# Performance work log

Measured on AMD Instinct MI355X. Metric: run time of the kernel, lower is better.

Reference implementation:

```python
import jax, jax.numpy as jnp
import numpy as np
from jax import lax

CHAR_SIZE, EMBED, HID = 20000, 128, 256
B, T = 256, 512


def setup_inputs() -> dict:
    key = jax.random.key(0)
    ks = jax.random.split(key, 12)
    s = 0.02
    return {
        "inputs": jax.random.randint(ks[0], (B, T), 0, CHAR_SIZE, dtype=jnp.int32),
        "input_end": jax.random.randint(ks[1], (B,), 0, B, dtype=jnp.int32),
        "embed_table": jax.random.normal(ks[2], (CHAR_SIZE, EMBED), jnp.float32) * s,
        "Wf": jax.random.normal(ks[3], (EMBED, 4 * HID), jnp.float32) * s,
        "Uf": jax.random.normal(ks[4], (HID, 4 * HID), jnp.float32) * s,
        "bf": jnp.zeros((4 * HID,), jnp.float32),
        "Wb": jax.random.normal(ks[5], (EMBED, 4 * HID), jnp.float32) * s,
        "Ub": jax.random.normal(ks[6], (HID, 4 * HID), jnp.float32) * s,
        "bb": jnp.zeros((4 * HID,), jnp.float32),
        "cls_W": jax.random.normal(ks[7], (2 * HID, 1), jnp.float32) * s,
        "cls_b": jnp.zeros((1,), jnp.float32),
        "ent_W": jax.random.normal(ks[8], (2 * HID, 3), jnp.float32) * s,
        "ent_b": jnp.zeros((3,), jnp.float32),
    }


def _masked_lstm(x_tbe, m_tb, W, U, b, reverse):
    """Keras-style masked LSTM; returns final hidden state [B, H].
    Masked steps carry (h, c) through unchanged."""
    Bn = x_tbe.shape[1]
    H = U.shape[0]

    def step(carry, inp):
        h, c = carry
        xt, mt = inp  # xt: [B,E], mt: [B]
        z = xt @ W + h @ U + b  # [B, 4H]
        i, f, g, o = jnp.split(z, 4, axis=-1)
        c_new = jax.nn.sigmoid(f) * c + jax.nn.sigmoid(i) * jnp.tanh(g)
        h_new = jax.nn.sigmoid(o) * jnp.tanh(c_new)
        m = mt[:, None]
        return (jnp.where(m, h_new, h), jnp.where(m, c_new, c)), None

    init = (jnp.zeros((Bn, H), x_tbe.dtype), jnp.zeros((Bn, H), x_tbe.dtype))
    (h, _), _ = lax.scan(step, init, (x_tbe, m_tb), reverse=reverse)
    return h


def reference(inputs, input_end, embed_table, Wf, Uf, bf, Wb, Ub, bb,
              cls_W, cls_b, ent_W, ent_b):
    mask = inputs > 0  # [B, T]
    embed = embed_table[inputs]  # [B, T, E]
    x_tbe = jnp.swapaxes(embed, 0, 1)  # [T, B, E]
    m_tb = mask.T  # [T, B]
    h_fwd = _masked_lstm(x_tbe, m_tb, Wf, Uf, bf, reverse=False)  # [B, H]
    h_bwd = _masked_lstm(x_tbe, m_tb, Wb, Ub, bb, reverse=True)   # [B, H]
    bivalue = jnp.concatenate([h_fwd, h_bwd], axis=-1)  # [B, 2H]
    sentence_end = bivalue[input_end]  # gather along batch axis, as in the original
    classifier_logits = jax.nn.sigmoid(sentence_end @ cls_W + cls_b)  # [B, 1]
    entity_logits = jax.nn.softmax(bivalue @ ent_W + ent_b, axis=-1)  # [B, 3]
    return classifier_logits, entity_logits
```

## Files before the change

kernel.cpp:

```cpp
#include <hip/hip_runtime.h>
#include <hip/hip_bf16.h>
#include <hip/hip_cooperative_groups.h>

#define EMBED 128
#define HID   256
#define BB    256
#define TT    512
#define G4    1024

typedef __attribute__((ext_vector_type(8))) short short8;
typedef __attribute__((ext_vector_type(4))) float f32x4;

#define OFF_WUP   0
#define SZ_WUP    (2*8*4*32*384*2)
#define OFF_BP    (OFF_WUP + SZ_WUP)
#define SZ_BP     (2*8*4*32*4)
#define OFF_XHAT  (OFF_BP + SZ_BP)
#define SZ_XHAT   ((size_t)BB*TT*EMBED*2)
#define OFF_HBUF  (OFF_XHAT + SZ_XHAT)
#define SZ_HBUF   (2*2*BB*HID*2)
#define OFF_HFIN  (OFF_HBUF + SZ_HBUF)
#define SZ_HFIN   (2*BB*HID*4)
#define OFF_FLAGS (OFF_HFIN + SZ_HFIN)
#define SZ_FLAGS  (2*8*8*4*64*4)
#define OFF_XCD   (OFF_FLAGS + SZ_FLAGS)
#define SZ_XCD    (128*16*4)

#define SPIN_GUARD (1 << 14)
#define HS_GUARD   (1 << 20)

__global__ void pack_kernel(const float* __restrict__ Wf, const float* __restrict__ Uf,
                            const float* __restrict__ bf,
                            const float* __restrict__ Wb, const float* __restrict__ Ub,
                            const float* __restrict__ bb,
                            __hip_bfloat16* __restrict__ WUp, float* __restrict__ bp) {
    int flat = blockIdx.x * 256 + threadIdx.x;
    int k = flat % 384;
    int rest = flat / 384;
    int jc   = rest & 31;
    int gate = (rest >> 5) & 3;
    int jg   = (rest >> 7) & 7;
    int dir  = rest >> 10;
    int J = gate * 256 + jg * 32 + jc;
    const float* W = dir ? Wb : Wf;
    const float* U = dir ? Ub : Uf;
    float v = (k < 128) ? W[(size_t)k * G4 + J] : U[(size_t)(k - 128) * G4 + J];
    WUp[flat] = __float2bfloat16(v);
    if (k == 0) {
        const float* bias = dir ? bb : bf;
        bp[rest] = bias[J];
    }
}

__global__ void gather_kernel(const int* __restrict__ inputs, const float* __restrict__ embed,
                              __hip_bfloat16* __restrict__ xhat) {
    int row = blockIdx.x * 2 + (threadIdx.x >> 7);
    int col = threadIdx.x & 127;
    int tok = inputs[row];
    xhat[(size_t)row * EMBED + col] = __float2bfloat16(embed[(size_t)tok * EMBED + col]);
}

__global__ void preclean_kernel() {
    if (threadIdx.x == 0) {
        asm volatile("buffer_wbl2 sc1\n\t"
                     "s_waitcnt vmcnt(0)\n\t"
                     "buffer_inv sc1\n\t"
                     "s_waitcnt vmcnt(0)" ::: "memory");
    }
}

__global__ void init_flags_kernel(int* __restrict__ p) {
    int i = blockIdx.x * 256 + threadIdx.x;
    int* q = p + i;
    unsigned z = 0;
    asm volatile("global_store_dword %0, %1, off sc0 sc1" :: "v"(q), "v"(z) : "memory");
}

__device__ __forceinline__ float frcp(float x) {
    float r;
    asm("v_rcp_f32 %0, %1" : "=v"(r) : "v"(x));
    return r;
}
__device__ __forceinline__ float sigf(float x)  { return frcp(1.f + __expf(-x)); }
__device__ __forceinline__ float ftanh(float x) { return 2.f * frcp(1.f + __expf(-2.f * x)) - 1.f; }

template<bool FAST>
__device__ __forceinline__ void lstm_loop(
        int dir, int jg, int bg, int wid, int lane,
        const int* __restrict__ inputs, const short* __restrict__ xrow,
        short* __restrict__ hbufs, int* __restrict__ flags,
        const short8 (*wfrag)[12], const float* bias,
        float* c_st, float* h_st, int brow0, int mrow0, int l15, int lhi, int jch) {

    const int rh = wid >> 1;
    int* myflag = flags + ((((dir * 8 + jg) * 8 + bg) * 4) + wid) * 64;
    const int l16 = lane & 15;
    int* pollp = flags + ((((dir * 8 + (l16 >> 1)) * 8 + bg) * 4) + (2 * rh + (l16 & 1))) * 64;

    const int   dstep = dir ? -1 : 1;
    const short* xptr = xrow + (size_t)(dir ? (TT - 1) : 0) * EMBED + 8 * lhi;
    const int*  mkp   = inputs + (size_t)brow0 * TT + (dir ? (TT - 1) : 0);
    const int*  mkp2  = mkp + 2 * TT;
    const short* hrd0 = hbufs + (size_t)(dir * 2) * BB * HID
                      + (size_t)(mrow0 + l15) * HID + 8 * lhi;
    const short* hrd1 = hrd0 + BB * HID;
    short* hwr0 = hbufs + (size_t)(dir * 2) * BB * HID
                + (size_t)brow0 * HID + jg * 32 + jch * 16 + l15;
    short* hwr1 = hwr0 + BB * HID;

    short8 xf[4];
    int mk_cur[4], mk_nxt[4];
#pragma unroll
    for (int kt = 0; kt < 4; ++kt)
        xf[kt] = *(const short8*)(xptr + kt * 32);
    mk_cur[0] = mkp[0]; mk_cur[1] = mkp[TT]; mk_cur[2] = mkp2[0]; mk_cur[3] = mkp2[TT];
    xptr += dstep * EMBED; mkp += dstep; mkp2 += dstep;

    for (int s = 0; s < TT; ++s) {
        int fv = 0;
        if (s != 0) {
            if constexpr (FAST) {
                asm volatile("global_load_dword %0, %1, off sc1"
                             : "=v"(fv) : "v"(pollp) : "memory");
            } else {
                asm volatile("global_load_dword %0, %1, off sc0 sc1"
                             : "=v"(fv) : "v"(pollp) : "memory");
            }
        }

        f32x4 acc[4];
#pragma unroll
        for (int g = 0; g < 4; ++g) {
            acc[g][0] = bias[g]; acc[g][1] = bias[g]; acc[g][2] = bias[g]; acc[g][3] = bias[g];
        }
#pragma unroll
        for (int kt = 0; kt < 4; ++kt)
#pragma unroll
            for (int g = 0; g < 4; ++g)
                acc[g] = __builtin_amdgcn_mfma_f32_16x16x32_bf16(xf[kt], wfrag[g][kt], acc[g], 0, 0, 0);

        if (s != 0) {
            asm volatile("s_waitcnt vmcnt(0)" : "+v"(fv) :: "memory");
            {
                int guard = 0;
                while (__any(fv < s)) {
                    if (++guard > SPIN_GUARD) break;
                    if constexpr (FAST) {
                        asm volatile("global_load_dword %0, %1, off sc1\n\t"
                                     "s_waitcnt vmcnt(0)"
                                     : "=v"(fv) : "v"(pollp) : "memory");
                    } else {
                        asm volatile("global_load_dword %0, %1, off sc0 sc1\n\t"
                                     "s_waitcnt vmcnt(0)"
                                     : "=v"(fv) : "v"(pollp) : "memory");
                    }
                }
            }

            short8 hf[8];
            const short* hbase = (s & 1) ? hrd1 : hrd0;
            if constexpr (FAST) {
                asm volatile(
                    "global_load_dwordx4 %0, %8, off sc1\n\t"
                    "global_load_dwordx4 %1, %8, off offset:64 sc1\n\t"
                    "global_load_dwordx4 %2, %8, off offset:128 sc1\n\t"
                    "global_load_dwordx4 %3, %8, off offset:192 sc1\n\t"
                    "global_load_dwordx4 %4, %8, off offset:256 sc1\n\t"
                    "global_load_dwordx4 %5, %8, off offset:320 sc1\n\t"
                    "global_load_dwordx4 %6, %8, off offset:384 sc1\n\t"
                    "global_load_dwordx4 %7, %8, off offset:448 sc1\n\t"
                    "s_waitcnt vmcnt(0)"
                    : "=&v"(hf[0]), "=&v"(hf[1]), "=&v"(hf[2]), "=&v"(hf[3]),
                      "=&v"(hf[4]), "=&v"(hf[5]), "=&v"(hf[6]), "=&v"(hf[7])
                    : "v"(hbase) : "memory");
            } else {
                asm volatile(
                    "global_load_dwordx4 %0, %8, off sc0 sc1\n\t"
                    "global_load_dwordx4 %1, %8, off offset:64 sc0 sc1\n\t"
                    "global_load_dwordx4 %2, %8, off offset:128 sc0 sc1\n\t"
                    "global_load_dwordx4 %3, %8, off offset:192 sc0 sc1\n\t"
                    "global_load_dwordx4 %4, %8, off offset:256 sc0 sc1\n\t"
                    "global_load_dwordx4 %5, %8, off offset:320 sc0 sc1\n\t"
                    "global_load_dwordx4 %6, %8, off offset:384 sc0 sc1\n\t"
                    "global_load_dwordx4 %7, %8, off offset:448 sc0 sc1\n\t"
                    "s_waitcnt vmcnt(0)"
                    : "=&v"(hf[0]), "=&v"(hf[1]), "=&v"(hf[2]), "=&v"(hf[3]),
                      "=&v"(hf[4]), "=&v"(hf[5]), "=&v"(hf[6]), "=&v"(hf[7])
                    : "v"(hbase) : "memory");
            }
            __builtin_amdgcn_sched_barrier(0);

#pragma unroll
            for (int kt = 0; kt < 8; ++kt)
#pragma unroll
                for (int g = 0; g < 4; ++g)
                    acc[g] = __builtin_amdgcn_mfma_f32_16x16x32_bf16(hf[kt], wfrag[g][kt + 4], acc[g], 0, 0, 0);
        }

        unsigned hv16[4];
#pragma unroll
        for (int r = 0; r < 4; ++r) {
            float zi = acc[0][r];
            float zf = acc[1][r];
            float zg = acc[2][r];
            float zo = acc[3][r];
            float cn = sigf(zf) * c_st[r] + sigf(zi) * ftanh(zg);
            float hn = sigf(zo) * ftanh(cn);
            if (mk_cur[r] > 0) { c_st[r] = cn; h_st[r] = hn; }
            __hip_bfloat16 hbf = __float2bfloat16(h_st[r]);
            hv16[r] = (unsigned)(*(unsigned short*)&hbf);
        }

        {
            const short* sb = ((s + 1) & 1) ? hwr1 : hwr0;
            if constexpr (FAST) {
                asm volatile(
                    "global_store_short %4, %0, off sc0\n\t"
                    "global_store_short %4, %1, off offset:512 sc0\n\t"
                    "global_store_short %4, %2, off offset:1024 sc0\n\t"
                    "global_store_short %4, %3, off offset:1536 sc0\n\t"
                    "s_waitcnt vmcnt(0)"
                    :: "v"(hv16[0]), "v"(hv16[1]), "v"(hv16[2]), "v"(hv16[3]), "v"(sb)
                    : "memory");
                if (lane == 0) {
                    int val = s + 1;
                    asm volatile("global_store_dword %0, %1, off sc0"
                                 :: "v"(myflag), "v"(val) : "memory");
                }
            } else {
                asm volatile(
                    "global_store_short %4, %0, off sc0 sc1\n\t"
                    "global_store_short %4, %1, off offset:512 sc0 sc1\n\t"
                    "global_store_short %4, %2, off offset:1024 sc0 sc1\n\t"
                    "global_store_short %4, %3, off offset:1536 sc0 sc1\n\t"
                    "s_waitcnt vmcnt(0)"
                    :: "v"(hv16[0]), "v"(hv16[1]), "v"(hv16[2]), "v"(hv16[3]), "v"(sb)
                    : "memory");
                if (lane == 0) {
                    int val = s + 1;
                    asm volatile("global_store_dword %0, %1, off sc0 sc1"
                                 :: "v"(myflag), "v"(val) : "memory");
                }
            }
        }

        if (s + 1 < TT) {
#pragma unroll
            for (int kt = 0; kt < 4; ++kt)
                xf[kt] = *(const short8*)(xptr + kt * 32);
            mk_nxt[0] = mkp[0]; mk_nxt[1] = mkp[TT];
            mk_nxt[2] = mkp2[0]; mk_nxt[3] = mkp2[TT];
            xptr += dstep * EMBED; mkp += dstep; mkp2 += dstep;
#pragma unroll
            for (int r = 0; r < 4; ++r) mk_cur[r] = mk_nxt[r];
        }
    }
}

__launch_bounds__(256, 1)
__global__ void lstm_kernel(const int* __restrict__ inputs,
                            const __hip_bfloat16* __restrict__ xhat,
                            const __hip_bfloat16* __restrict__ WUp,
                            const float* __restrict__ bp,
                            __hip_bfloat16* __restrict__ hbuf,
                            float* __restrict__ hfinal,
                            int* __restrict__ flags,
                            int* __restrict__ xcdtab) {
    const int bid = blockIdx.x;
    const int jg  = bid >> 4;
    const int dir = (bid >> 3) & 1;
    const int bg  = bid & 7;
    const int tid = threadIdx.x;
    const int wid = tid >> 6;
    const int lane = tid & 63;
    const int l15 = lane & 15, lhi = lane >> 4;
    const int jch = wid & 1;
    const int mrow0 = bg * 32 + (wid >> 1) * 16;
    const int brow0 = mrow0 + 4 * lhi;

    short8 wfrag[4][12];
    const short* wu = (const short*)WUp + (size_t)(dir * 8 + jg) * 4 * 32 * 384;
#pragma unroll
    for (int g = 0; g < 4; ++g)
#pragma unroll
        for (int kt = 0; kt < 12; ++kt)
            wfrag[g][kt] = *(const short8*)(wu + (size_t)(g * 32 + jch * 16 + l15) * 384 + kt * 32 + 8 * lhi);

    float bias[4];
#pragma unroll
    for (int g = 0; g < 4; ++g)
        bias[g] = bp[((dir * 8 + jg) * 4 + g) * 32 + jch * 16 + l15];

    int myxcd;
    asm volatile("s_getreg_b32 %0, hwreg(HW_REG_XCC_ID)" : "=s"(myxcd));
    if (tid == 0) {
        int* mp = xcdtab + bid * 16;
        int pv = 0x100 | myxcd;
        asm volatile("global_store_dword %0, %1, off sc0 sc1" :: "v"(mp), "v"(pv) : "memory");
    }
    int fast;
    {
        const int l8 = lane & 7;
        int* pp = xcdtab + ((l8 * 16) + dir * 8 + bg) * 16;
        int e, guard = 0;
        do {
            asm volatile("global_load_dword %0, %1, off sc0 sc1\n\t"
                         "s_waitcnt vmcnt(0)"
                         : "=v"(e) : "v"(pp) : "memory");
            if (++guard > HS_GUARD) break;
        } while (__any(e == 0));
        fast = (__all(e == (0x100 | myxcd))) ? 1 : 0;
    }

    float c_st[4] = {0, 0, 0, 0};
    float h_st[4] = {0, 0, 0, 0};
    const short* xrow = (const short*)xhat + (size_t)(mrow0 + l15) * TT * EMBED;
    short* hbufs = (short*)hbuf;

    if (fast)
        lstm_loop<true>(dir, jg, bg, wid, lane, inputs, xrow, hbufs, flags,
                        wfrag, bias, c_st, h_st, brow0, mrow0, l15, lhi, jch);
    else
        lstm_loop<false>(dir, jg, bg, wid, lane, inputs, xrow, hbufs, flags,
                         wfrag, bias, c_st, h_st, brow0, mrow0, l15, lhi, jch);

#pragma unroll
    for (int r = 0; r < 4; ++r)
        hfinal[((size_t)dir * BB + brow0 + r) * HID + jg * 32 + jch * 16 + l15] = h_st[r];
}

__global__ void epilogue_kernel(const int* __restrict__ input_end,
                                const float* __restrict__ hfinal,
                                const float* __restrict__ cls_W, const float* __restrict__ cls_b,
                                const float* __restrict__ ent_W, const float* __restrict__ ent_b,
                                float* __restrict__ out) {
    int b = blockIdx.x;
    int lane = threadIdx.x;
    int ie = input_end[b];
    float pe0 = 0, pe1 = 0, pe2 = 0, pc = 0;
    for (int k = lane; k < 2 * HID; k += 64) {
        float bv, se;
        if (k < HID) {
            bv = hfinal[(size_t)b * HID + k];
            se = hfinal[(size_t)ie * HID + k];
        } else {
            bv = hfinal[(size_t)(BB + b) * HID + (k - HID)];
            se = hfinal[(size_t)(BB + ie) * HID + (k - HID)];
        }
        pe0 += bv * ent_W[k * 3 + 0];
        pe1 += bv * ent_W[k * 3 + 1];
        pe2 += bv * ent_W[k * 3 + 2];
        pc  += se * cls_W[k];
    }
    for (int off = 32; off; off >>= 1) {
        pe0 += __shfl_down(pe0, off);
        pe1 += __shfl_down(pe1, off);
        pe2 += __shfl_down(pe2, off);
        pc  += __shfl_down(pc, off);
    }
    if (lane == 0) {
        float l0 = pe0 + ent_b[0], l1 = pe1 + ent_b[1], l2 = pe2 + ent_b[2];
        float m = fmaxf(l0, fmaxf(l1, l2));
        float e0 = __expf(l0 - m), e1 = __expf(l1 - m), e2 = __expf(l2 - m);
        float ssum = e0 + e1 + e2;
        out[256 + b * 3 + 0] = e0 / ssum;
        out[256 + b * 3 + 1] = e1 / ssum;
        out[256 + b * 3 + 2] = e2 / ssum;
        float cl = pc + cls_b[0];
        out[b] = 1.f / (1.f + __expf(-cl));
    }
}

extern "C" void kernel_launch(void* const* d_in, const int* in_sizes, int n_in,
                              void* d_out, int out_size, void* d_ws, size_t ws_size,
                              hipStream_t stream) {
    const int*   inputs    = (const int*)d_in[0];
    const int*   input_end = (const int*)d_in[1];
    const float* embed     = (const float*)d_in[2];
    const float* Wf        = (const float*)d_in[3];
    const float* Uf        = (const float*)d_in[4];
    const float* bf        = (const float*)d_in[5];
    const float* Wb        = (const float*)d_in[6];
    const float* Ub        = (const float*)d_in[7];
    const float* bb        = (const float*)d_in[8];
    const float* cls_W     = (const float*)d_in[9];
    const float* cls_b     = (const float*)d_in[10];
    const float* ent_W     = (const float*)d_in[11];
    const float* ent_b     = (const float*)d_in[12];
    float* out = (float*)d_out;

    char* ws = (char*)d_ws;
    __hip_bfloat16* WUp    = (__hip_bfloat16*)(ws + OFF_WUP);
    float*          bp     = (float*)(ws + OFF_BP);
    __hip_bfloat16* xhat   = (__hip_bfloat16*)(ws + OFF_XHAT);
    __hip_bfloat16* hbuf   = (__hip_bfloat16*)(ws + OFF_HBUF);
    float*          hfinal = (float*)(ws + OFF_HFIN);
    int*            flags  = (int*)(ws + OFF_FLAGS);
    int*            xcdtab = (int*)(ws + OFF_XCD);

    preclean_kernel<<<64, 64, 0, stream>>>();
    init_flags_kernel<<<136, 256, 0, stream>>>(flags);
    pack_kernel<<<3072, 256, 0, stream>>>(Wf, Uf, bf, Wb, Ub, bb, WUp, bp);
    gather_kernel<<<BB * TT / 2, 256, 0, stream>>>(inputs, embed, xhat);

    void* args[] = {(void*)&inputs, (void*)&xhat, (void*)&WUp, (void*)&bp,
                    (void*)&hbuf, (void*)&hfinal, (void*)&flags, (void*)&xcdtab};
    hipLaunchCooperativeKernel((void*)lstm_kernel, dim3(128), dim3(256), args, 0, stream);

    epilogue_kernel<<<BB, 64, 0, stream>>>(input_end, hfinal, cls_W, cls_b, ent_W, ent_b, out);
}
```

Baseline: 1.188 ms.

## Software-pipeline LSTM step: precompute next input projection and prefetch two steps ahead

Restructures the recurrent loop into a manually unrolled two-step body with ping-pong input buffers. After publishing h for step s, each wave issues the flag poll and prefetches the x tile and mask for step s+2, then computes the x@W MFMA part for step s+1 before waiting. This takes the input projection and the global x/mask loads off the critical path between the flag wait and the h-load. In exchange it keeps more registers live and relies on careful vmcnt accounting (vmcnt(8)) to stay correct.

```diff
diff --git a/kernel.cpp b/kernel.cpp
--- a/kernel.cpp
+++ b/kernel.cpp
@@ -85,6 +85,164 @@
 __device__ __forceinline__ float ftanh(float x) { return 2.f * frcp(1.f + __expf(-2.f * x)) - 1.f; }
 
 template<bool FAST>
+__device__ __forceinline__ void lstm_body(
+        int s, short8 (&PF)[4], short8 (&MM)[4], int& fv, f32x4 (&acc)[4],
+        int* mk_cur, int* mk_nxt, float* c_st, float* h_st,
+        const short*& xptr, const int*& mkp, const int*& mkp2, int dstep,
+        int* pollp, int* myflag,
+        const short* hrd0, const short* hrd1, short* hwr0, short* hwr1,
+        const short8 (*wfrag)[12], const float* bias) {
+
+    if (s != 0) {
+        if (s == TT - 1)
+            asm volatile("s_waitcnt vmcnt(0)" : "+v"(fv) :: "memory");
+        else
+            asm volatile("s_waitcnt vmcnt(8)" : "+v"(fv) :: "memory");
+        __builtin_amdgcn_sched_barrier(0);
+        {
+            int guard = 0;
+            while (__any(fv < s)) {
+                if (++guard > SPIN_GUARD) break;
+                if constexpr (FAST)
+                    asm volatile("global_load_dword %0, %1, off sc1\n\t"
+                                 "s_waitcnt vmcnt(0)"
+                                 : "=&v"(fv) : "v"(pollp) : "memory");
+                else
+                    asm volatile("global_load_dword %0, %1, off sc0 sc1\n\t"
+                                 "s_waitcnt vmcnt(0)"
+                                 : "=&v"(fv) : "v"(pollp) : "memory");
+            }
+        }
+
+        short8 hf[8];
+        const short* hbase = (s & 1) ? hrd1 : hrd0;
+        if constexpr (FAST) {
+            asm volatile(
+                "global_load_dwordx4 %0, %8, off sc1\n\t"
+                "global_load_dwordx4 %1, %8, off offset:64 sc1\n\t"
+                "global_load_dwordx4 %2, %8, off offset:128 sc1\n\t"
+                "global_load_dwordx4 %3, %8, off offset:192 sc1\n\t"
+                "global_load_dwordx4 %4, %8, off offset:256 sc1\n\t"
+                "global_load_dwordx4 %5, %8, off offset:320 sc1\n\t"
+                "global_load_dwordx4 %6, %8, off offset:384 sc1\n\t"
+                "global_load_dwordx4 %7, %8, off offset:448 sc1\n\t"
+                "s_waitcnt vmcnt(0)"
+                : "=&v"(hf[0]), "=&v"(hf[1]), "=&v"(hf[2]), "=&v"(hf[3]),
+                  "=&v"(hf[4]), "=&v"(hf[5]), "=&v"(hf[6]), "=&v"(hf[7])
+                : "v"(hbase) : "memory");
+        } else {
+            asm volatile(
+                "global_load_dwordx4 %0, %8, off sc0 sc1\n\t"
+                "global_load_dwordx4 %1, %8, off offset:64 sc0 sc1\n\t"
+                "global_load_dwordx4 %2, %8, off offset:128 sc0 sc1\n\t"
+                "global_load_dwordx4 %3, %8, off offset:192 sc0 sc1\n\t"
+                "global_load_dwordx4 %4, %8, off offset:256 sc0 sc1\n\t"
+                "global_load_dwordx4 %5, %8, off offset:320 sc0 sc1\n\t"
+                "global_load_dwordx4 %6, %8, off offset:384 sc0 sc1\n\t"
+                "global_load_dwordx4 %7, %8, off offset:448 sc0 sc1\n\t"
+                "s_waitcnt vmcnt(0)"
+                : "=&v"(hf[0]), "=&v"(hf[1]), "=&v"(hf[2]), "=&v"(hf[3]),
+                  "=&v"(hf[4]), "=&v"(hf[5]), "=&v"(hf[6]), "=&v"(hf[7])
+                : "v"(hbase) : "memory");
+        }
+        __builtin_amdgcn_sched_barrier(0);
+
+#pragma unroll
+        for (int kt = 0; kt < 8; ++kt)
+#pragma unroll
+            for (int g = 0; g < 4; ++g)
+                acc[g] = __builtin_amdgcn_mfma_f32_16x16x32_bf16(hf[kt], wfrag[g][kt + 4], acc[g], 0, 0, 0);
+    }
+
+    unsigned hv16[4];
+#pragma unroll
+    for (int r = 0; r < 4; ++r) {
+        float zi = acc[0][r];
+        float zf = acc[1][r];
+        float zg = acc[2][r];
+        float zo = acc[3][r];
+        float cn = sigf(zf) * c_st[r] + sigf(zi) * ftanh(zg);
+        float hn = sigf(zo) * ftanh(cn);
+        if (mk_cur[r] > 0) { c_st[r] = cn; h_st[r] = hn; }
+        __hip_bfloat16 hbf = __float2bfloat16(h_st[r]);
+        hv16[r] = (unsigned)(*(unsigned short*)&hbf);
+    }
+#pragma unroll
+    for (int r = 0; r < 4; ++r) mk_cur[r] = mk_nxt[r];
+
+    {
+        const short* sb = ((s + 1) & 1) ? hwr1 : hwr0;
+        if constexpr (FAST) {
+            asm volatile(
+                "global_store_short %4, %0, off sc0\n\t"
+                "global_store_short %4, %1, off offset:512 sc0\n\t"
+                "global_store_short %4, %2, off offset:1024 sc0\n\t"
+                "global_store_short %4, %3, off offset:1536 sc0\n\t"
+                "s_waitcnt vmcnt(0)"
+                :: "v"(hv16[0]), "v"(hv16[1]), "v"(hv16[2]), "v"(hv16[3]), "v"(sb)
+                : "memory");
+            if ((threadIdx.x & 63) == 0) {
+                int val = s + 1;
+                asm volatile("global_store_dword %0, %1, off sc0"
+                             :: "v"(myflag), "v"(val) : "memory");
+            }
+        } else {
+            asm volatile(
+                "global_store_short %4, %0, off sc0 sc1\n\t"
+                "global_store_short %4, %1, off offset:512 sc0 sc1\n\t"
+                "global_store_short %4, %2, off offset:1024 sc0 sc1\n\t"
+                "global_store_short %4, %3, off offset:1536 sc0 sc1\n\t"
+                "s_waitcnt vmcnt(0)"
+                :: "v"(hv16[0]), "v"(hv16[1]), "v"(hv16[2]), "v"(hv16[3]), "v"(sb)
+                : "memory");
+            if ((threadIdx.x & 63) == 0) {
+                int val = s + 1;
+                asm volatile("global_store_dword %0, %1, off sc0 sc1"
+                             :: "v"(myflag), "v"(val) : "memory");
+            }
+        }
+    }
+    __builtin_amdgcn_sched_barrier(0);
+
+    if (s + 1 < TT) {
+        if constexpr (FAST)
+            asm volatile("global_load_dword %0, %1, off sc1"
+                         : "=&v"(fv) : "v"(pollp) : "memory");
+        else
+            asm volatile("global_load_dword %0, %1, off sc0 sc1"
+                         : "=&v"(fv) : "v"(pollp) : "memory");
+
+        if (s + 2 < TT) {
+            asm volatile(
+                "global_load_dwordx4 %0, %8, off\n\t"
+                "global_load_dwordx4 %1, %8, off offset:64\n\t"
+                "global_load_dwordx4 %2, %8, off offset:128\n\t"
+                "global_load_dwordx4 %3, %8, off offset:192\n\t"
+                "global_load_dword %4, %9, off\n\t"
+                "global_load_dword %5, %9, off offset:2048\n\t"
+                "global_load_dword %6, %10, off\n\t"
+                "global_load_dword %7, %10, off offset:2048"
+                : "=&v"(PF[0]), "=&v"(PF[1]), "=&v"(PF[2]), "=&v"(PF[3]),
+                  "=&v"(mk_nxt[0]), "=&v"(mk_nxt[1]), "=&v"(mk_nxt[2]), "=&v"(mk_nxt[3])
+                : "v"(xptr), "v"(mkp), "v"(mkp2)
+                : "memory");
+            xptr += dstep * EMBED; mkp += dstep; mkp2 += dstep;
+        }
+        __builtin_amdgcn_sched_barrier(0);
+
+#pragma unroll
+        for (int g = 0; g < 4; ++g) {
+            acc[g][0] = bias[g]; acc[g][1] = bias[g]; acc[g][2] = bias[g]; acc[g][3] = bias[g];
+        }
+#pragma unroll
+        for (int kt = 0; kt < 4; ++kt)
+#pragma unroll
+            for (int g = 0; g < 4; ++g)
+                acc[g] = __builtin_amdgcn_mfma_f32_16x16x32_bf16(MM[kt], wfrag[g][kt], acc[g], 0, 0, 0);
+    }
+}
+
+template<bool FAST>
 __device__ __forceinline__ void lstm_loop(
         int dir, int jg, int bg, int wid, int lane,
         const int* __restrict__ inputs, const short* __restrict__ xrow,
@@ -108,152 +266,37 @@
                 + (size_t)brow0 * HID + jg * 32 + jch * 16 + l15;
     short* hwr1 = hwr0 + BB * HID;
 
-    short8 xf[4];
+    short8 xfA[4], xfB[4];
     int mk_cur[4], mk_nxt[4];
-#pragma unroll
-    for (int kt = 0; kt < 4; ++kt)
-        xf[kt] = *(const short8*)(xptr + kt * 32);
+    f32x4 acc[4];
+    int fv = 0;
+
+#pragma unroll
+    for (int kt = 0; kt < 4; ++kt) xfA[kt] = *(const short8*)(xptr + kt * 32);
     mk_cur[0] = mkp[0]; mk_cur[1] = mkp[TT]; mk_cur[2] = mkp2[0]; mk_cur[3] = mkp2[TT];
     xptr += dstep * EMBED; mkp += dstep; mkp2 += dstep;
-
-    for (int s = 0; s < TT; ++s) {
-        int fv = 0;
-        if (s != 0) {
-            if constexpr (FAST) {
-                asm volatile("global_load_dword %0, %1, off sc1"
-                             : "=v"(fv) : "v"(pollp) : "memory");
-            } else {
-                asm volatile("global_load_dword %0, %1, off sc0 sc1"
-                             : "=v"(fv) : "v"(pollp) : "memory");
-            }
-        }
-
-        f32x4 acc[4];
-#pragma unroll
-        for (int g = 0; g < 4; ++g) {
-            acc[g][0] = bias[g]; acc[g][1] = bias[g]; acc[g][2] = bias[g]; acc[g][3] = bias[g];
-        }
-#pragma unroll
-        for (int kt = 0; kt < 4; ++kt)
-#pragma unroll
-            for (int g = 0; g < 4; ++g)
-                acc[g] = __builtin_amdgcn_mfma_f32_16x16x32_bf16(xf[kt], wfrag[g][kt], acc[g], 0, 0, 0);
-
-        if (s != 0) {
-            asm volatile("s_waitcnt vmcnt(0)" : "+v"(fv) :: "memory");
-            {
-                int guard = 0;
-                while (__any(fv < s)) {
-                    if (++guard > SPIN_GUARD) break;
-                    if constexpr (FAST) {
-                        asm volatile("global_load_dword %0, %1, off sc1\n\t"
-                                     "s_waitcnt vmcnt(0)"
-                                     : "=v"(fv) : "v"(pollp) : "memory");
-                    } else {
-                        asm volatile("global_load_dword %0, %1, off sc0 sc1\n\t"
-                                     "s_waitcnt vmcnt(0)"
-                                     : "=v"(fv) : "v"(pollp) : "memory");
-                    }
-                }
-            }
-
-            short8 hf[8];
-            const short* hbase = (s & 1) ? hrd1 : hrd0;
-            if constexpr (FAST) {
-                asm volatile(
-                    "global_load_dwordx4 %0, %8, off sc1\n\t"
-                    "global_load_dwordx4 %1, %8, off offset:64 sc1\n\t"
-                    "global_load_dwordx4 %2, %8, off offset:128 sc1\n\t"
-                    "global_load_dwordx4 %3, %8, off offset:192 sc1\n\t"
-                    "global_load_dwordx4 %4, %8, off offset:256 sc1\n\t"
-                    "global_load_dwordx4 %5, %8, off offset:320 sc1\n\t"
-                    "global_load_dwordx4 %6, %8, off offset:384 sc1\n\t"
-                    "global_load_dwordx4 %7, %8, off offset:448 sc1\n\t"
-                    "s_waitcnt vmcnt(0)"
-                    : "=&v"(hf[0]), "=&v"(hf[1]), "=&v"(hf[2]), "=&v"(hf[3]),
-                      "=&v"(hf[4]), "=&v"(hf[5]), "=&v"(hf[6]), "=&v"(hf[7])
-                    : "v"(hbase) : "memory");
-            } else {
-                asm volatile(
-                    "global_load_dwordx4 %0, %8, off sc0 sc1\n\t"
-                    "global_load_dwordx4 %1, %8, off offset:64 sc0 sc1\n\t"
-                    "global_load_dwordx4 %2, %8, off offset:128 sc0 sc1\n\t"
-                    "global_load_dwordx4 %3, %8, off offset:192 sc0 sc1\n\t"
-                    "global_load_dwordx4 %4, %8, off offset:256 sc0 sc1\n\t"
-                    "global_load_dwordx4 %5, %8, off offset:320 sc0 sc1\n\t"
-                    "global_load_dwordx4 %6, %8, off offset:384 sc0 sc1\n\t"
-                    "global_load_dwordx4 %7, %8, off offset:448 sc0 sc1\n\t"
-                    "s_waitcnt vmcnt(0)"
-                    : "=&v"(hf[0]), "=&v"(hf[1]), "=&v"(hf[2]), "=&v"(hf[3]),
-                      "=&v"(hf[4]), "=&v"(hf[5]), "=&v"(hf[6]), "=&v"(hf[7])
-                    : "v"(hbase) : "memory");
-            }
-            __builtin_amdgcn_sched_barrier(0);
-
-#pragma unroll
-            for (int kt = 0; kt < 8; ++kt)
-#pragma unroll
-                for (int g = 0; g < 4; ++g)
-                    acc[g] = __builtin_amdgcn_mfma_f32_16x16x32_bf16(hf[kt], wfrag[g][kt + 4], acc[g], 0, 0, 0);
-        }
-
-        unsigned hv16[4];
-#pragma unroll
-        for (int r = 0; r < 4; ++r) {
-            float zi = acc[0][r];
-            float zf = acc[1][r];
-            float zg = acc[2][r];
-            float zo = acc[3][r];
-            float cn = sigf(zf) * c_st[r] + sigf(zi) * ftanh(zg);
-            float hn = sigf(zo) * ftanh(cn);
-            if (mk_cur[r] > 0) { c_st[r] = cn; h_st[r] = hn; }
-            __hip_bfloat16 hbf = __float2bfloat16(h_st[r]);
-            hv16[r] = (unsigned)(*(unsigned short*)&hbf);
-        }
-
-        {
-            const short* sb = ((s + 1) & 1) ? hwr1 : hwr0;
-            if constexpr (FAST) {
-                asm volatile(
-                    "global_store_short %4, %0, off sc0\n\t"
-                    "global_store_short %4, %1, off offset:512 sc0\n\t"
-                    "global_store_short %4, %2, off offset:1024 sc0\n\t"
-                    "global_store_short %4, %3, off offset:1536 sc0\n\t"
-                    "s_waitcnt vmcnt(0)"
-                    :: "v"(hv16[0]), "v"(hv16[1]), "v"(hv16[2]), "v"(hv16[3]), "v"(sb)
-                    : "memory");
-                if (lane == 0) {
-                    int val = s + 1;
-                    asm volatile("global_store_dword %0, %1, off sc0"
-                                 :: "v"(myflag), "v"(val) : "memory");
-                }
-            } else {
-                asm volatile(
-                    "global_store_short %4, %0, off sc0 sc1\n\t"
-                    "global_store_short %4, %1, off offset:512 sc0 sc1\n\t"
-                    "global_store_short %4, %2, off offset:1024 sc0 sc1\n\t"
-                    "global_store_short %4, %3, off offset:1536 sc0 sc1\n\t"
-                    "s_waitcnt vmcnt(0)"
-                    :: "v"(hv16[0]), "v"(hv16[1]), "v"(hv16[2]), "v"(hv16[3]), "v"(sb)
-                    : "memory");
-                if (lane == 0) {
-                    int val = s + 1;
-                    asm volatile("global_store_dword %0, %1, off sc0 sc1"
-                                 :: "v"(myflag), "v"(val) : "memory");
-                }
-            }
-        }
-
-        if (s + 1 < TT) {
-#pragma unroll
-            for (int kt = 0; kt < 4; ++kt)
-                xf[kt] = *(const short8*)(xptr + kt * 32);
-            mk_nxt[0] = mkp[0]; mk_nxt[1] = mkp[TT];
-            mk_nxt[2] = mkp2[0]; mk_nxt[3] = mkp2[TT];
-            xptr += dstep * EMBED; mkp += dstep; mkp2 += dstep;
-#pragma unroll
-            for (int r = 0; r < 4; ++r) mk_cur[r] = mk_nxt[r];
-        }
+#pragma unroll
+    for (int kt = 0; kt < 4; ++kt) xfB[kt] = *(const short8*)(xptr + kt * 32);
+    mk_nxt[0] = mkp[0]; mk_nxt[1] = mkp[TT]; mk_nxt[2] = mkp2[0]; mk_nxt[3] = mkp2[TT];
+    xptr += dstep * EMBED; mkp += dstep; mkp2 += dstep;
+
+#pragma unroll
+    for (int g = 0; g < 4; ++g) {
+        acc[g][0] = bias[g]; acc[g][1] = bias[g]; acc[g][2] = bias[g]; acc[g][3] = bias[g];
+    }
+#pragma unroll
+    for (int kt = 0; kt < 4; ++kt)
+#pragma unroll
+        for (int g = 0; g < 4; ++g)
+            acc[g] = __builtin_amdgcn_mfma_f32_16x16x32_bf16(xfA[kt], wfrag[g][kt], acc[g], 0, 0, 0);
+
+    for (int s2 = 0; s2 < TT; s2 += 2) {
+        lstm_body<FAST>(s2,     xfA, xfB, fv, acc, mk_cur, mk_nxt, c_st, h_st,
+                        xptr, mkp, mkp2, dstep, pollp, myflag,
+                        hrd0, hrd1, hwr0, hwr1, wfrag, bias);
+        lstm_body<FAST>(s2 + 1, xfB, xfA, fv, acc, mk_cur, mk_nxt, c_st, h_st,
+                        xptr, mkp, mkp2, dstep, pollp, myflag,
+                        hrd0, hrd1, hwr0, hwr1, wfrag, bias);
     }
 }
 
```

New measurement: 1.164 ms. -2.0%, faster.
